# Kernel tuning notes

Measured on AMD Instinct MI355X. Metric: run time of the kernel, lower is better.

The kernel has to match this reference:

```python
import jax, jax.numpy as jnp
import numpy as np

N = 100000
E = 1600000
D_IN = 128
D_HID = 128
D_HID2 = D_HID // 2  # 64
D_OUT = 1


def _glorot(key, shape):
    fan_in, fan_out = shape[1], shape[0]
    lim = float(np.sqrt(6.0 / (fan_in + fan_out)))
    return jax.random.uniform(key, shape, jnp.float32, -lim, lim)


def setup_inputs() -> dict:
    key = jax.random.key(0)
    ks = jax.random.split(key, 10)
    x = jax.random.normal(ks[0], (N, D_IN), jnp.float32)
    edge_index = jax.random.randint(ks[1], (2, E), 0, N, jnp.int64)
    return {
        "x": x,
        "edge_index": edge_index,
        # SAGEConv1: lin_l acts on mean-aggregated neighbors, lin_r on root
        "W1_l": _glorot(ks[2], (D_HID, D_IN)),
        "W1_r": _glorot(ks[3], (D_HID, D_IN)),
        "b1": jnp.zeros((D_HID,), jnp.float32),
        # SAGEConv2
        "W2_l": _glorot(ks[4], (D_HID2, D_HID)),
        "W2_r": _glorot(ks[5], (D_HID2, D_HID)),
        "b2": jnp.zeros((D_HID2,), jnp.float32),
        # classifier Linear
        "Wc": _glorot(ks[6], (D_OUT, D_HID2)),
        "bc": jnp.zeros((D_OUT,), jnp.float32),
    }


def _sage_conv(x, src, dst, Wl, Wr, b):
    # mean aggregation of source features onto destination nodes
    msg = x[src]  # [E, d] gather
    agg = jax.ops.segment_sum(msg, dst, num_segments=x.shape[0])  # [N, d]
    deg = jax.ops.segment_sum(jnp.ones((src.shape[0],), x.dtype), dst,
                              num_segments=x.shape[0])  # [N]
    agg = agg / jnp.maximum(deg, 1.0)[:, None]
    # out = lin_l(mean_aggr) + lin_r(x) + bias  (PyG SAGEConv default)
    return agg @ Wl.T + x @ Wr.T + b


def reference(x, edge_index, W1_l, W1_r, b1, W2_l, W2_r, b2, Wc, bc):
    src, dst = edge_index[0], edge_index[1]
    h = jax.nn.relu(_sage_conv(x, src, dst, W1_l, W1_r, b1))
    # dropout(p=0.3) is identity in eval mode
    h = jax.nn.relu(_sage_conv(h, src, dst, W2_l, W2_r, b2))
    logits = h @ Wc.T + bc  # [N, 1]
    return logits
```

## Files before the change

kernel.cpp:

```cpp
#include <hip/hip_runtime.h>


static constexpr int TPB = 256;
static constexpr int NWG = 512;
static constexpr int ECMAX = 3200;
static constexpr int NBMAX = 1024;

typedef __attribute__((ext_vector_type(8))) short bf16x8;
typedef __attribute__((ext_vector_type(4))) float f32x4;
typedef __attribute__((ext_vector_type(2))) float f32x2;

#if __has_builtin(__builtin_amdgcn_cvt_pk_f32_fp8) && __has_builtin(__builtin_amdgcn_cvt_pk_fp8_f32)
#define FP8_HW 1
#endif

__device__ __forceinline__ unsigned short f2bf(float f) {
  union { float f; unsigned u; } v; v.f = f;
  unsigned r = v.u + 0x7FFFu + ((v.u >> 16) & 1u);
  return (unsigned short)(r >> 16);
}
__device__ __forceinline__ float bf2f(unsigned short h) {
  union { unsigned u; float f; } v; v.u = ((unsigned)h) << 16;
  return v.f;
}

__device__ __forceinline__ float fp82f_sw(unsigned u) {
  unsigned e = (u >> 3) & 15u, m = u & 7u;
  float f;
  if (e == 0) f = (float)m * 0.001953125f;
  else {
    union { unsigned u; float f; } v;
    v.u = ((e + 120u) << 23) | (m << 20);
    f = v.f;
  }
  return (u & 0x80u) ? -f : f;
}

__device__ __forceinline__ unsigned char f2fp8(float f) {
#ifdef FP8_HW
  return (unsigned char)(__builtin_amdgcn_cvt_pk_fp8_f32(f, f, 0, false) & 0xFF);
#else
  union { float f; unsigned u; } v; v.f = f;
  unsigned s = (v.u >> 24) & 0x80u;
  unsigned a = v.u & 0x7FFFFFFFu;
  if (a >= 0x43E00000u) return (unsigned char)(s | 0x7Eu);
  int e32 = (int)(a >> 23);
  if (e32 < 121) {
    float sc = __builtin_fabsf(f) * 512.0f;
    int m = (int)(sc + 0.5f);
    if (m >= 8) return (unsigned char)(s | 0x08u);
    return (unsigned char)(s | (unsigned)m);
  }
  unsigned m = a & 0x7FFFFFu;
  unsigned lsb = (m >> 20) & 1u;
  m += 0x7FFFFu + lsb;
  unsigned e8 = (unsigned)(e32 - 120);
  if (m >= 0x800000u) { m -= 0x800000u; e8 += 1; }
  if (e8 >= 16) return (unsigned char)(s | 0x7Eu);
  return (unsigned char)(s | (e8 << 3) | (m >> 20));
#endif
}

__device__ __forceinline__ void fp8x8_acc(uint2 v, float* acc) {
#ifdef FP8_HW
  f32x2 a0 = __builtin_amdgcn_cvt_pk_f32_fp8(v.x, false);
  f32x2 a1 = __builtin_amdgcn_cvt_pk_f32_fp8(v.x, true);
  f32x2 a2 = __builtin_amdgcn_cvt_pk_f32_fp8(v.y, false);
  f32x2 a3 = __builtin_amdgcn_cvt_pk_f32_fp8(v.y, true);
  acc[0] += a0[0]; acc[1] += a0[1]; acc[2] += a1[0]; acc[3] += a1[1];
  acc[4] += a2[0]; acc[5] += a2[1]; acc[6] += a3[0]; acc[7] += a3[1];
#else
  acc[0] += fp82f_sw(v.x & 255); acc[1] += fp82f_sw((v.x >> 8) & 255);
  acc[2] += fp82f_sw((v.x >> 16) & 255); acc[3] += fp82f_sw(v.x >> 24);
  acc[4] += fp82f_sw(v.y & 255); acc[5] += fp82f_sw((v.y >> 8) & 255);
  acc[6] += fp82f_sw((v.y >> 16) & 255); acc[7] += fp82f_sw(v.y >> 24);
#endif
}

__global__ __launch_bounds__(TPB) void k_bcount(const int* __restrict__ dst,
                                                int* __restrict__ bcnt,
                                                int E, int NB, int EC) {
  extern __shared__ int lhist0[];
  int t = threadIdx.x;
  for (int b = t; b < NB; b += TPB) lhist0[b] = 0;
  __syncthreads();
  int base = blockIdx.x * EC;
  int cnt = min(EC, E - base);
  for (int i = t; i < cnt; i += TPB)
    atomicAdd(&lhist0[dst[base + i] >> 7], 1);
  __syncthreads();
  for (int b = t; b < NB; b += TPB) {
    int c = lhist0[b];
    if (c) atomicAdd(&bcnt[b], c);
  }
}

__global__ __launch_bounds__(TPB) void k_bscatter(
    const int* __restrict__ src, const int* __restrict__ dst,
    const int* __restrict__ bcnt, int* __restrict__ bcur,
    int* __restrict__ ebuf, int E, int NB, int EC) {
  __shared__ int pv[ECMAX];
  __shared__ unsigned short kb[ECMAX];
  __shared__ int sb[NBMAX];
  __shared__ int lhist[NBMAX];
  __shared__ int lcur[NBMAX];
  __shared__ int sp[TPB];
  int t = threadIdx.x;
  int loc[4]; int ssum = 0;
#pragma unroll
  for (int q = 0; q < 4; ++q) {
    int idx = t * 4 + q;
    loc[q] = (idx < NB) ? bcnt[idx] : 0;
    ssum += loc[q];
  }
  sp[t] = ssum; __syncthreads();
  for (int off = 1; off < TPB; off <<= 1) {
    int x = (t >= off) ? sp[t - off] : 0;
    __syncthreads();
    sp[t] += x;
    __syncthreads();
  }
  int run = sp[t] - ssum;
#pragma unroll
  for (int q = 0; q < 4; ++q) {
    int idx = t * 4 + q;
    if (idx < NB) sb[idx] = run;
    run += loc[q];
  }
  for (int b = t; b < NB; b += TPB) lhist[b] = 0;
  int base = blockIdx.x * EC;
  int cnt = min(EC, E - base);
  __syncthreads();
  for (int i = t; i < cnt; i += TPB) {
    int sv = src[base + i], dv = dst[base + i];
    int b = dv >> 7;
    kb[i] = (unsigned short)b;
    pv[i] = ((dv & 127) << 17) | sv;
    atomicAdd(&lhist[b], 1);
  }
  __syncthreads();
  for (int b = t; b < NB; b += TPB) {
    int c = lhist[b];
    lcur[b] = c ? (sb[b] + atomicAdd(&bcur[b], c)) : 0;
  }
  __syncthreads();
  for (int i = t; i < cnt; i += TPB) {
    int b = kb[i];
    int pos = atomicAdd(&lcur[b], 1);
    ebuf[pos] = pv[i];
  }
}

__global__ __launch_bounds__(TPB) void k_bcsr(
    const int* __restrict__ ebuf, const int* __restrict__ bcnt,
    int* __restrict__ rowptr, int* __restrict__ col, int N, int NB) {
  __shared__ int deg[128], sscan[128], lcur[128], red[TPB];
  int b = blockIdx.x, t = threadIdx.x;
  int part = 0;
  for (int i = t; i < b; i += TPB) part += bcnt[i];
  red[t] = part; __syncthreads();
  for (int off = TPB / 2; off > 0; off >>= 1) {
    if (t < off) red[t] += red[t + off];
    __syncthreads();
  }
  int e0 = red[0];
  int e1 = e0 + bcnt[b];
  if (t < 128) deg[t] = 0;
  __syncthreads();
  for (int i = e0 + t; i < e1; i += TPB)
    atomicAdd(&deg[ebuf[i] >> 17], 1);
  __syncthreads();
  if (t < 128) sscan[t] = deg[t];
  __syncthreads();
  for (int off = 1; off < 128; off <<= 1) {
    int x = 0;
    if (t < 128 && t >= off) x = sscan[t - off];
    __syncthreads();
    if (t < 128) sscan[t] += x;
    __syncthreads();
  }
  if (t < 128) {
    int excl = sscan[t] - deg[t];
    int node0 = (b << 7) + t;
    if (node0 < N) rowptr[node0] = e0 + excl;
    lcur[t] = e0 + excl;
  }
  if (b == NB - 1 && t == 0) rowptr[N] = e1;
  __syncthreads();
  for (int i = e0 + t; i < e1; i += TPB) {
    int pvv = ebuf[i];
    int pos = atomicAdd(&lcur[pvv >> 17], 1);
    col[pos] = pvv & 0x1FFFF;
  }
}

static constexpr int LD = 136;

template <bool OUT8>
__device__ __forceinline__ void mfma_tile_128(
    const unsigned short* As, const unsigned short* Bs,
    void* __restrict__ outp, int row0, int N, int w, int l) {
  int lr = l & 15, lk = l >> 4;
  f32x4 acc[4][2];
#pragma unroll
  for (int mb = 0; mb < 4; ++mb)
#pragma unroll
    for (int nb = 0; nb < 2; ++nb)
#pragma unroll
      for (int q = 0; q < 4; ++q) acc[mb][nb][q] = 0.f;
#pragma unroll
  for (int ks = 0; ks < 4; ++ks) {
    int koff = ks * 32 + lk * 8;
    bf16x8 a[4], bfr[2];
#pragma unroll
    for (int mb = 0; mb < 4; ++mb)
      a[mb] = *(const bf16x8*)&As[(mb * 16 + lr) * LD + koff];
#pragma unroll
    for (int nb = 0; nb < 2; ++nb)
      bfr[nb] = *(const bf16x8*)&Bs[(w * 32 + nb * 16 + lr) * LD + koff];
#pragma unroll
    for (int mb = 0; mb < 4; ++mb)
#pragma unroll
      for (int nb = 0; nb < 2; ++nb)
        acc[mb][nb] = __builtin_amdgcn_mfma_f32_16x16x32_bf16(a[mb], bfr[nb], acc[mb][nb], 0, 0, 0);
  }
#pragma unroll
  for (int mb = 0; mb < 4; ++mb) {
    int r = row0 + mb * 16 + lk * 4;
#pragma unroll
    for (int nb = 0; nb < 2; ++nb) {
      int c = w * 32 + nb * 16 + lr;
#pragma unroll
      for (int j = 0; j < 4; ++j) {
        if (r + j < N) {
          if (OUT8) ((unsigned char*)outp)[(size_t)(r + j) * 128 + c] = f2fp8(acc[mb][nb][j]);
          else      ((unsigned short*)outp)[(size_t)(r + j) * 128 + c] = f2bf(acc[mb][nb][j]);
        }
      }
    }
  }
}

__global__ __launch_bounds__(TPB) void k_lin1d(
    const float* __restrict__ X, const float* __restrict__ W1l,
    const float* __restrict__ W1r, unsigned char* __restrict__ t1,
    unsigned short* __restrict__ r1, int N) {
  __shared__ unsigned short Bs[128 * LD];
  __shared__ unsigned short As[64 * LD];
  int t = threadIdx.x;
  int row0 = blockIdx.x * 64;
  for (int i = t; i < 64 * 32; i += TPB) {
    int r = i >> 5, k4 = i & 31;
    int gr = row0 + r;
    float4 v;
    if (gr < N) v = *(const float4*)&X[(size_t)gr * 128 + k4 * 4];
    else { v.x = v.y = v.z = v.w = 0.f; }
    ushort4 o; o.x = f2bf(v.x); o.y = f2bf(v.y); o.z = f2bf(v.z); o.w = f2bf(v.w);
    *(ushort4*)&As[r * LD + k4 * 4] = o;
  }
  for (int i = t; i < 128 * 32; i += TPB) {
    int r = i >> 5, k4 = i & 31;
    float4 v = *(const float4*)&W1l[r * 128 + k4 * 4];
    ushort4 o; o.x = f2bf(v.x); o.y = f2bf(v.y); o.z = f2bf(v.z); o.w = f2bf(v.w);
    *(ushort4*)&Bs[r * LD + k4 * 4] = o;
  }
  __syncthreads();
  int w = t >> 6, l = t & 63;
  mfma_tile_128<true>(As, Bs, t1, row0, N, w, l);
  __syncthreads();
  for (int i = t; i < 128 * 32; i += TPB) {
    int r = i >> 5, k4 = i & 31;
    float4 v = *(const float4*)&W1r[r * 128 + k4 * 4];
    ushort4 o; o.x = f2bf(v.x); o.y = f2bf(v.y); o.z = f2bf(v.z); o.w = f2bf(v.w);
    *(ushort4*)&Bs[r * LD + k4 * 4] = o;
  }
  __syncthreads();
  mfma_tile_128<false>(As, Bs, r1, row0, N, w, l);
}

__global__ void k_aggh1(const unsigned char* __restrict__ t1,
                        const unsigned short* __restrict__ r1,
                        const int* __restrict__ rowptr, const int* __restrict__ col,
                        const float* __restrict__ b1,
                        unsigned short* __restrict__ h1, int n) {
  int wid = (int)(((size_t)blockIdx.x * blockDim.x + threadIdx.x) >> 6);
  int l = threadIdx.x & 63;
  if (wid >= n) return;
  int rp0 = rowptr[wid], rp1 = rowptr[wid + 1];
  int g = l >> 4, s = l & 15;
  float acc[8];
#pragma unroll
  for (int q = 0; q < 8; ++q) acc[q] = 0.f;
  int j = rp0 + g;
  for (; j + 12 < rp1; j += 16) {
    int c0 = col[j], c1 = col[j + 4], c2 = col[j + 8], c3 = col[j + 12];
    uint2 v0 = *(const uint2*)&t1[(size_t)c0 * 128 + s * 8];
    uint2 v1 = *(const uint2*)&t1[(size_t)c1 * 128 + s * 8];
    uint2 v2 = *(const uint2*)&t1[(size_t)c2 * 128 + s * 8];
    uint2 v3 = *(const uint2*)&t1[(size_t)c3 * 128 + s * 8];
    fp8x8_acc(v0, acc); fp8x8_acc(v1, acc);
    fp8x8_acc(v2, acc); fp8x8_acc(v3, acc);
  }
  for (; j + 4 < rp1; j += 8) {
    int c0 = col[j], c1 = col[j + 4];
    uint2 v0 = *(const uint2*)&t1[(size_t)c0 * 128 + s * 8];
    uint2 v1 = *(const uint2*)&t1[(size_t)c1 * 128 + s * 8];
    fp8x8_acc(v0, acc); fp8x8_acc(v1, acc);
  }
  if (j < rp1) {
    uint2 v0 = *(const uint2*)&t1[(size_t)col[j] * 128 + s * 8];
    fp8x8_acc(v0, acc);
  }
#pragma unroll
  for (int q = 0; q < 8; ++q) {
    acc[q] += __shfl_xor(acc[q], 16, 64);
    acc[q] += __shfl_xor(acc[q], 32, 64);
  }
  if (g == 0) {
    int d = rp1 - rp0;
    float inv = 1.f / (float)(d > 1 ? d : 1);
    bf16x8 rr = *(const bf16x8*)&r1[(size_t)wid * 128 + s * 8];
    float4 bb0 = *(const float4*)&b1[s * 8];
    float4 bb1 = *(const float4*)&b1[s * 8 + 4];
    float bbv[8] = {bb0.x, bb0.y, bb0.z, bb0.w, bb1.x, bb1.y, bb1.z, bb1.w};
    bf16x8 o;
#pragma unroll
    for (int q = 0; q < 8; ++q) {
      float h = acc[q] * inv + bf2f((unsigned short)rr[q]) + bbv[q];
      h = h > 0.f ? h : 0.f;
      o[q] = (short)f2bf(h);
    }
    *(bf16x8*)&h1[(size_t)wid * 128 + s * 8] = o;
  }
}

__global__ __launch_bounds__(TPB) void k_lin2(
    const unsigned short* __restrict__ h1,
    const float* __restrict__ W2l, const float* __restrict__ W2r,
    unsigned char* __restrict__ y2, unsigned short* __restrict__ r2, int N) {
  __shared__ unsigned short Bs[128 * LD];
  __shared__ unsigned short As[64 * LD];
  int t = threadIdx.x;
  for (int i = t; i < 128 * 32; i += TPB) {
    int r = i >> 5, k4 = i & 31;
    const float* srcp = (r < 64) ? &W2l[(size_t)r * 128 + k4 * 4]
                                 : &W2r[(size_t)(r - 64) * 128 + k4 * 4];
    float4 v = *(const float4*)srcp;
    ushort4 o; o.x = f2bf(v.x); o.y = f2bf(v.y); o.z = f2bf(v.z); o.w = f2bf(v.w);
    *(ushort4*)&Bs[r * LD + k4 * 4] = o;
  }
  int row0 = blockIdx.x * 64;
  for (int i = t * 8; i < 64 * 128; i += TPB * 8) {
    int r = i >> 7, k8 = i & 127;
    int gr = row0 + r;
    bf16x8 v;
    if (gr < N) v = *(const bf16x8*)&h1[(size_t)gr * 128 + k8];
    else { for (int q = 0; q < 8; ++q) v[q] = 0; }
    *(bf16x8*)&As[r * LD + k8] = v;
  }
  __syncthreads();
  int w = t >> 6, l = t & 63;
  int lr = l & 15, lk = l >> 4;
  f32x4 acc[4][2];
#pragma unroll
  for (int mb = 0; mb < 4; ++mb)
#pragma unroll
    for (int nb = 0; nb < 2; ++nb)
#pragma unroll
      for (int q = 0; q < 4; ++q) acc[mb][nb][q] = 0.f;
#pragma unroll
  for (int ks = 0; ks < 4; ++ks) {
    int koff = ks * 32 + lk * 8;
    bf16x8 a[4], bfr[2];
#pragma unroll
    for (int mb = 0; mb < 4; ++mb)
      a[mb] = *(const bf16x8*)&As[(mb * 16 + lr) * LD + koff];
#pragma unroll
    for (int nb = 0; nb < 2; ++nb)
      bfr[nb] = *(const bf16x8*)&Bs[(w * 32 + nb * 16 + lr) * LD + koff];
#pragma unroll
    for (int mb = 0; mb < 4; ++mb)
#pragma unroll
      for (int nb = 0; nb < 2; ++nb)
        acc[mb][nb] = __builtin_amdgcn_mfma_f32_16x16x32_bf16(a[mb], bfr[nb], acc[mb][nb], 0, 0, 0);
  }
#pragma unroll
  for (int mb = 0; mb < 4; ++mb) {
    int r = row0 + mb * 16 + lk * 4;
#pragma unroll
    for (int nb = 0; nb < 2; ++nb) {
      int c = w * 32 + nb * 16 + lr;
#pragma unroll
      for (int j = 0; j < 4; ++j) {
        if (r + j < N) {
          if (c < 64) y2[(size_t)(r + j) * 64 + c] = f2fp8(acc[mb][nb][j]);
          else        r2[(size_t)(r + j) * 64 + (c - 64)] = f2bf(acc[mb][nb][j]);
        }
      }
    }
  }
}

__global__ void k_agghead(const unsigned char* __restrict__ y2,
                          const unsigned short* __restrict__ r2,
                          const int* __restrict__ rowptr, const int* __restrict__ col,
                          const float* __restrict__ b2, const float* __restrict__ Wc,
                          const float* __restrict__ bc, float* __restrict__ out, int n) {
  int wid = (int)(((size_t)blockIdx.x * blockDim.x + threadIdx.x) >> 6);
  int l = threadIdx.x & 63;
  if (wid >= n) return;
  int rp0 = rowptr[wid], rp1 = rowptr[wid + 1];
  int g = l >> 3, s = l & 7;
  float acc[8];
#pragma unroll
  for (int q = 0; q < 8; ++q) acc[q] = 0.f;
  int j = rp0 + g;
  for (; j + 8 < rp1; j += 16) {
    int c0 = col[j], c1 = col[j + 8];
    uint2 v0 = *(const uint2*)&y2[(size_t)c0 * 64 + s * 8];
    uint2 v1 = *(const uint2*)&y2[(size_t)c1 * 64 + s * 8];
    fp8x8_acc(v0, acc); fp8x8_acc(v1, acc);
  }
  if (j < rp1) {
    uint2 v0 = *(const uint2*)&y2[(size_t)col[j] * 64 + s * 8];
    fp8x8_acc(v0, acc);
  }
#pragma unroll
  for (int q = 0; q < 8; ++q) {
    acc[q] += __shfl_xor(acc[q], 8, 64);
    acc[q] += __shfl_xor(acc[q], 16, 64);
    acc[q] += __shfl_xor(acc[q], 32, 64);
  }
  if (g == 0) {
    int d = rp1 - rp0;
    float inv = 1.f / (float)(d > 1 ? d : 1);
    bf16x8 rr = *(const bf16x8*)&r2[(size_t)wid * 64 + s * 8];
    float4 bb0 = *(const float4*)&b2[s * 8];
    float4 bb1 = *(const float4*)&b2[s * 8 + 4];
    float bbv[8] = {bb0.x, bb0.y, bb0.z, bb0.w, bb1.x, bb1.y, bb1.z, bb1.w};
    float4 wc0 = *(const float4*)&Wc[s * 8];
    float4 wc1 = *(const float4*)&Wc[s * 8 + 4];
    float wcv[8] = {wc0.x, wc0.y, wc0.z, wc0.w, wc1.x, wc1.y, wc1.z, wc1.w};
    float p = 0.f;
#pragma unroll
    for (int q = 0; q < 8; ++q) {
      float h = acc[q] * inv + bf2f((unsigned short)rr[q]) + bbv[q];
      h = h > 0.f ? h : 0.f;
      p += h * wcv[q];
    }
    p += __shfl_xor(p, 1, 64);
    p += __shfl_xor(p, 2, 64);
    p += __shfl_xor(p, 4, 64);
    if (s == 0) out[wid] = p + bc[0];
  }
}

extern "C" void kernel_launch(void* const* d_in, const int* in_sizes, int n_in,
                              void* d_out, int out_size, void* d_ws, size_t ws_size,
                              hipStream_t stream) {
  const float* x   = (const float*)d_in[0];
  const int*   ei  = (const int*)d_in[1];
  const float* W1l = (const float*)d_in[2];
  const float* W1r = (const float*)d_in[3];
  const float* b1  = (const float*)d_in[4];
  const float* W2l = (const float*)d_in[5];
  const float* W2r = (const float*)d_in[6];
  const float* b2  = (const float*)d_in[7];
  const float* Wc  = (const float*)d_in[8];
  const float* bc  = (const float*)d_in[9];
  float* logits = (float*)d_out;

  const int N = in_sizes[0] / 128;
  const int E = in_sizes[1] / 2;
  const int NB = (N + 127) >> 7;
  const int EC = (E + NWG - 1) / NWG;

  char* ws = (char*)d_ws;
  size_t o = 0;
  auto alloc = [&](size_t bytes) { size_t r = o; o += (bytes + 511) & ~511ULL; return r; };
  size_t o_rp    = alloc((size_t)(N + 1) * 4);
  size_t o_bcc   = alloc((size_t)(2 * NB) * 4);
  size_t o_col   = alloc((size_t)E * 4);
  size_t o_ebuf  = alloc((size_t)E * 4);
  size_t o_t1    = alloc((size_t)N * 128);
  size_t o_r1    = alloc((size_t)N * 128 * 2);
  size_t o_h1    = alloc((size_t)N * 128 * 2);
  size_t o_y2    = alloc((size_t)N * 64);
  size_t o_r2    = alloc((size_t)N * 64 * 2);
  if (o > ws_size) return;

  int* rp    = (int*)(ws + o_rp);
  int* bcnt  = (int*)(ws + o_bcc);
  int* bcur  = bcnt + NB;
  int* col   = (int*)(ws + o_col);
  int* ebuf  = (int*)(ws + o_ebuf);
  unsigned char*  t1 = (unsigned char*)(ws + o_t1);
  unsigned short* r1 = (unsigned short*)(ws + o_r1);
  unsigned short* h1 = (unsigned short*)(ws + o_h1);
  unsigned char*  y2 = (unsigned char*)(ws + o_y2);
  unsigned short* r2 = (unsigned short*)(ws + o_r2);

  const int* esrc = ei;
  const int* edst = ei + E;

  int gtiles = (N + 63) / 64;
  int nodeblocks = (int)(((size_t)N * 64 + TPB - 1) / TPB);

  hipMemsetAsync(bcnt, 0, (size_t)(2 * NB) * 4, stream);
  k_bcount<<<NWG, TPB, (size_t)NB * 4, stream>>>(edst, bcnt, E, NB, EC);
  k_lin1d<<<gtiles, TPB, 0, stream>>>(x, W1l, W1r, t1, r1, N);
  k_bscatter<<<NWG, TPB, 0, stream>>>(esrc, edst, bcnt, bcur, ebuf, E, NB, EC);
  k_bcsr<<<NB, TPB, 0, stream>>>(ebuf, bcnt, rp, col, N, NB);
  k_aggh1<<<nodeblocks, TPB, 0, stream>>>(t1, r1, rp, col, b1, h1, N);
  k_lin2<<<gtiles, TPB, 0, stream>>>(h1, W2l, W2r, y2, r2, N);
  k_agghead<<<nodeblocks, TPB, 0, stream>>>(y2, r2, rp, col, b2, Wc, bc, logits, N);
}
```

Before: 227.0 us.

## Pre-convert weights to bf16 once and read B fragments from global

Adds a small prep kernel that converts all layer weights to bf16 once per call, instead of every GEMM block re-reading fp32 weights and converting them into shared memory. The lin1 and lin2 kernels drop the weight shared-memory tile and load B fragments straight from global/L2. lin1 also computes both projections in one pass over the A fragments, with two accumulator sets. This is meant to cut redundant per-block weight conversion and LDS traffic and raise occupancy, at the cost of one extra launch, more registers in lin1 and uncoalesced global fragment loads.

```diff
diff --git a/kernel.cpp b/kernel.cpp
--- a/kernel.cpp
+++ b/kernel.cpp
@@ -77,6 +77,18 @@
 #endif
 }
 
+__global__ void k_wprep(const float* __restrict__ W1l, const float* __restrict__ W1r,
+                        const float* __restrict__ W2l, const float* __restrict__ W2r,
+                        unsigned short* __restrict__ wb1l,
+                        unsigned short* __restrict__ wb1r,
+                        unsigned short* __restrict__ wb2) {
+  int i = blockIdx.x * blockDim.x + threadIdx.x;
+  if (i < 16384) wb1l[i] = f2bf(W1l[i]);
+  else if (i < 32768) wb1r[i - 16384] = f2bf(W1r[i - 16384]);
+  else if (i < 40960) wb2[i - 32768] = f2bf(W2l[i - 32768]);
+  else if (i < 49152) wb2[8192 + i - 40960] = f2bf(W2r[i - 40960]);
+}
+
 __global__ __launch_bounds__(TPB) void k_bcount(const int* __restrict__ dst,
                                                 int* __restrict__ bcnt,
                                                 int E, int NB, int EC) {
@@ -196,56 +208,10 @@
 
 static constexpr int LD = 136;
 
-template <bool OUT8>
-__device__ __forceinline__ void mfma_tile_128(
-    const unsigned short* As, const unsigned short* Bs,
-    void* __restrict__ outp, int row0, int N, int w, int l) {
-  int lr = l & 15, lk = l >> 4;
-  f32x4 acc[4][2];
-#pragma unroll
-  for (int mb = 0; mb < 4; ++mb)
-#pragma unroll
-    for (int nb = 0; nb < 2; ++nb)
-#pragma unroll
-      for (int q = 0; q < 4; ++q) acc[mb][nb][q] = 0.f;
-#pragma unroll
-  for (int ks = 0; ks < 4; ++ks) {
-    int koff = ks * 32 + lk * 8;
-    bf16x8 a[4], bfr[2];
-#pragma unroll
-    for (int mb = 0; mb < 4; ++mb)
-      a[mb] = *(const bf16x8*)&As[(mb * 16 + lr) * LD + koff];
-#pragma unroll
-    for (int nb = 0; nb < 2; ++nb)
-      bfr[nb] = *(const bf16x8*)&Bs[(w * 32 + nb * 16 + lr) * LD + koff];
-#pragma unroll
-    for (int mb = 0; mb < 4; ++mb)
-#pragma unroll
-      for (int nb = 0; nb < 2; ++nb)
-        acc[mb][nb] = __builtin_amdgcn_mfma_f32_16x16x32_bf16(a[mb], bfr[nb], acc[mb][nb], 0, 0, 0);
-  }
-#pragma unroll
-  for (int mb = 0; mb < 4; ++mb) {
-    int r = row0 + mb * 16 + lk * 4;
-#pragma unroll
-    for (int nb = 0; nb < 2; ++nb) {
-      int c = w * 32 + nb * 16 + lr;
-#pragma unroll
-      for (int j = 0; j < 4; ++j) {
-        if (r + j < N) {
-          if (OUT8) ((unsigned char*)outp)[(size_t)(r + j) * 128 + c] = f2fp8(acc[mb][nb][j]);
-          else      ((unsigned short*)outp)[(size_t)(r + j) * 128 + c] = f2bf(acc[mb][nb][j]);
-        }
-      }
-    }
-  }
-}
-
-__global__ __launch_bounds__(TPB) void k_lin1d(
-    const float* __restrict__ X, const float* __restrict__ W1l,
-    const float* __restrict__ W1r, unsigned char* __restrict__ t1,
+__global__ __launch_bounds__(TPB, 4) void k_lin1(
+    const float* __restrict__ X, const unsigned short* __restrict__ wl,
+    const unsigned short* __restrict__ wr, unsigned char* __restrict__ t1,
     unsigned short* __restrict__ r1, int N) {
-  __shared__ unsigned short Bs[128 * LD];
   __shared__ unsigned short As[64 * LD];
   int t = threadIdx.x;
   int row0 = blockIdx.x * 64;
@@ -258,24 +224,111 @@
     ushort4 o; o.x = f2bf(v.x); o.y = f2bf(v.y); o.z = f2bf(v.z); o.w = f2bf(v.w);
     *(ushort4*)&As[r * LD + k4 * 4] = o;
   }
-  for (int i = t; i < 128 * 32; i += TPB) {
-    int r = i >> 5, k4 = i & 31;
-    float4 v = *(const float4*)&W1l[r * 128 + k4 * 4];
-    ushort4 o; o.x = f2bf(v.x); o.y = f2bf(v.y); o.z = f2bf(v.z); o.w = f2bf(v.w);
-    *(ushort4*)&Bs[r * LD + k4 * 4] = o;
-  }
   __syncthreads();
   int w = t >> 6, l = t & 63;
-  mfma_tile_128<true>(As, Bs, t1, row0, N, w, l);
-  __syncthreads();
-  for (int i = t; i < 128 * 32; i += TPB) {
-    int r = i >> 5, k4 = i & 31;
-    float4 v = *(const float4*)&W1r[r * 128 + k4 * 4];
-    ushort4 o; o.x = f2bf(v.x); o.y = f2bf(v.y); o.z = f2bf(v.z); o.w = f2bf(v.w);
-    *(ushort4*)&Bs[r * LD + k4 * 4] = o;
-  }
-  __syncthreads();
-  mfma_tile_128<false>(As, Bs, r1, row0, N, w, l);
+  int lr = l & 15, lk = l >> 4;
+  f32x4 at[4][2], ar[4][2];
+#pragma unroll
+  for (int mb = 0; mb < 4; ++mb)
+#pragma unroll
+    for (int nb = 0; nb < 2; ++nb)
+#pragma unroll
+      for (int q = 0; q < 4; ++q) { at[mb][nb][q] = 0.f; ar[mb][nb][q] = 0.f; }
+#pragma unroll
+  for (int ks = 0; ks < 4; ++ks) {
+    int koff = ks * 32 + lk * 8;
+    bf16x8 a[4], bl[2], br[2];
+#pragma unroll
+    for (int mb = 0; mb < 4; ++mb)
+      a[mb] = *(const bf16x8*)&As[(mb * 16 + lr) * LD + koff];
+#pragma unroll
+    for (int nb = 0; nb < 2; ++nb) {
+      int c = w * 32 + nb * 16 + lr;
+      bl[nb] = *(const bf16x8*)&wl[c * 128 + koff];
+      br[nb] = *(const bf16x8*)&wr[c * 128 + koff];
+    }
+#pragma unroll
+    for (int mb = 0; mb < 4; ++mb)
+#pragma unroll
+      for (int nb = 0; nb < 2; ++nb) {
+        at[mb][nb] = __builtin_amdgcn_mfma_f32_16x16x32_bf16(a[mb], bl[nb], at[mb][nb], 0, 0, 0);
+        ar[mb][nb] = __builtin_amdgcn_mfma_f32_16x16x32_bf16(a[mb], br[nb], ar[mb][nb], 0, 0, 0);
+      }
+  }
+#pragma unroll
+  for (int mb = 0; mb < 4; ++mb) {
+    int r = row0 + mb * 16 + lk * 4;
+#pragma unroll
+    for (int nb = 0; nb < 2; ++nb) {
+      int c = w * 32 + nb * 16 + lr;
+#pragma unroll
+      for (int j = 0; j < 4; ++j) {
+        if (r + j < N) {
+          t1[(size_t)(r + j) * 128 + c] = f2fp8(at[mb][nb][j]);
+          r1[(size_t)(r + j) * 128 + c] = f2bf(ar[mb][nb][j]);
+        }
+      }
+    }
+  }
+}
+
+__global__ __launch_bounds__(TPB, 4) void k_lin2(
+    const unsigned short* __restrict__ h1, const unsigned short* __restrict__ w2,
+    unsigned char* __restrict__ y2, unsigned short* __restrict__ r2, int N) {
+  __shared__ unsigned short As[64 * LD];
+  int t = threadIdx.x;
+  int row0 = blockIdx.x * 64;
+  for (int i = t * 8; i < 64 * 128; i += TPB * 8) {
+    int r = i >> 7, k8 = i & 127;
+    int gr = row0 + r;
+    bf16x8 v;
+    if (gr < N) v = *(const bf16x8*)&h1[(size_t)gr * 128 + k8];
+    else { for (int q = 0; q < 8; ++q) v[q] = 0; }
+    *(bf16x8*)&As[r * LD + k8] = v;
+  }
+  __syncthreads();
+  int w = t >> 6, l = t & 63;
+  int lr = l & 15, lk = l >> 4;
+  f32x4 acc[4][2];
+#pragma unroll
+  for (int mb = 0; mb < 4; ++mb)
+#pragma unroll
+    for (int nb = 0; nb < 2; ++nb)
+#pragma unroll
+      for (int q = 0; q < 4; ++q) acc[mb][nb][q] = 0.f;
+#pragma unroll
+  for (int ks = 0; ks < 4; ++ks) {
+    int koff = ks * 32 + lk * 8;
+    bf16x8 a[4], bfr[2];
+#pragma unroll
+    for (int mb = 0; mb < 4; ++mb)
+      a[mb] = *(const bf16x8*)&As[(mb * 16 + lr) * LD + koff];
+#pragma unroll
+    for (int nb = 0; nb < 2; ++nb) {
+      int c = w * 32 + nb * 16 + lr;
+      bfr[nb] = *(const bf16x8*)&w2[c * 128 + koff];
+    }
+#pragma unroll
+    for (int mb = 0; mb < 4; ++mb)
+#pragma unroll
+      for (int nb = 0; nb < 2; ++nb)
+        acc[mb][nb] = __builtin_amdgcn_mfma_f32_16x16x32_bf16(a[mb], bfr[nb], acc[mb][nb], 0, 0, 0);
+  }
+#pragma unroll
+  for (int mb = 0; mb < 4; ++mb) {
+    int r = row0 + mb * 16 + lk * 4;
+#pragma unroll
+    for (int nb = 0; nb < 2; ++nb) {
+      int c = w * 32 + nb * 16 + lr;
+#pragma unroll
+      for (int j = 0; j < 4; ++j) {
+        if (r + j < N) {
+          if (c < 64) y2[(size_t)(r + j) * 64 + c] = f2fp8(acc[mb][nb][j]);
+          else        r2[(size_t)(r + j) * 64 + (c - 64)] = f2bf(acc[mb][nb][j]);
+        }
+      }
+    }
+  }
 }
 
 __global__ void k_aggh1(const unsigned char* __restrict__ t1,
@@ -331,73 +384,6 @@
       o[q] = (short)f2bf(h);
     }
     *(bf16x8*)&h1[(size_t)wid * 128 + s * 8] = o;
-  }
-}
-
-__global__ __launch_bounds__(TPB) void k_lin2(
-    const unsigned short* __restrict__ h1,
-    const float* __restrict__ W2l, const float* __restrict__ W2r,
-    unsigned char* __restrict__ y2, unsigned short* __restrict__ r2, int N) {
-  __shared__ unsigned short Bs[128 * LD];
-  __shared__ unsigned short As[64 * LD];
-  int t = threadIdx.x;
-  for (int i = t; i < 128 * 32; i += TPB) {
-    int r = i >> 5, k4 = i & 31;
-    const float* srcp = (r < 64) ? &W2l[(size_t)r * 128 + k4 * 4]
-                                 : &W2r[(size_t)(r - 64) * 128 + k4 * 4];
-    float4 v = *(const float4*)srcp;
-    ushort4 o; o.x = f2bf(v.x); o.y = f2bf(v.y); o.z = f2bf(v.z); o.w = f2bf(v.w);
-    *(ushort4*)&Bs[r * LD + k4 * 4] = o;
-  }
-  int row0 = blockIdx.x * 64;
-  for (int i = t * 8; i < 64 * 128; i += TPB * 8) {
-    int r = i >> 7, k8 = i & 127;
-    int gr = row0 + r;
-    bf16x8 v;
-    if (gr < N) v = *(const bf16x8*)&h1[(size_t)gr * 128 + k8];
-    else { for (int q = 0; q < 8; ++q) v[q] = 0; }
-    *(bf16x8*)&As[r * LD + k8] = v;
-  }
-  __syncthreads();
-  int w = t >> 6, l = t & 63;
-  int lr = l & 15, lk = l >> 4;
-  f32x4 acc[4][2];
-#pragma unroll
-  for (int mb = 0; mb < 4; ++mb)
-#pragma unroll
-    for (int nb = 0; nb < 2; ++nb)
-#pragma unroll
-      for (int q = 0; q < 4; ++q) acc[mb][nb][q] = 0.f;
-#pragma unroll
-  for (int ks = 0; ks < 4; ++ks) {
-    int koff = ks * 32 + lk * 8;
-    bf16x8 a[4], bfr[2];
-#pragma unroll
-    for (int mb = 0; mb < 4; ++mb)
-      a[mb] = *(const bf16x8*)&As[(mb * 16 + lr) * LD + koff];
-#pragma unroll
-    for (int nb = 0; nb < 2; ++nb)
-      bfr[nb] = *(const bf16x8*)&Bs[(w * 32 + nb * 16 + lr) * LD + koff];
-#pragma unroll
-    for (int mb = 0; mb < 4; ++mb)
-#pragma unroll
-      for (int nb = 0; nb < 2; ++nb)
-        acc[mb][nb] = __builtin_amdgcn_mfma_f32_16x16x32_bf16(a[mb], bfr[nb], acc[mb][nb], 0, 0, 0);
-  }
-#pragma unroll
-  for (int mb = 0; mb < 4; ++mb) {
-    int r = row0 + mb * 16 + lk * 4;
-#pragma unroll
-    for (int nb = 0; nb < 2; ++nb) {
-      int c = w * 32 + nb * 16 + lr;
-#pragma unroll
-      for (int j = 0; j < 4; ++j) {
-        if (r + j < N) {
-          if (c < 64) y2[(size_t)(r + j) * 64 + c] = f2fp8(acc[mb][nb][j]);
-          else        r2[(size_t)(r + j) * 64 + (c - 64)] = f2bf(acc[mb][nb][j]);
-        }
-      }
-    }
   }
 }
 
@@ -482,6 +468,7 @@
   size_t o_bcc   = alloc((size_t)(2 * NB) * 4);
   size_t o_col   = alloc((size_t)E * 4);
   size_t o_ebuf  = alloc((size_t)E * 4);
+  size_t o_wb    = alloc((size_t)(3 * 128 * 128) * 2);
   size_t o_t1    = alloc((size_t)N * 128);
   size_t o_r1    = alloc((size_t)N * 128 * 2);
   size_t o_h1    = alloc((size_t)N * 128 * 2);
@@ -494,6 +481,9 @@
   int* bcur  = bcnt + NB;
   int* col   = (int*)(ws + o_col);
   int* ebuf  = (int*)(ws + o_ebuf);
+  unsigned short* wb1l = (unsigned short*)(ws + o_wb);
+  unsigned short* wb1r = wb1l + 128 * 128;
+  unsigned short* wb2  = wb1r + 128 * 128;
   unsigned char*  t1 = (unsigned char*)(ws + o_t1);
   unsigned short* r1 = (unsigned short*)(ws + o_r1);
   unsigned short* h1 = (unsigned short*)(ws + o_h1);
@@ -507,11 +497,12 @@
   int nodeblocks = (int)(((size_t)N * 64 + TPB - 1) / TPB);
 
   hipMemsetAsync(bcnt, 0, (size_t)(2 * NB) * 4, stream);
+  k_wprep<<<192, TPB, 0, stream>>>(W1l, W1r, W2l, W2r, wb1l, wb1r, wb2);
   k_bcount<<<NWG, TPB, (size_t)NB * 4, stream>>>(edst, bcnt, E, NB, EC);
-  k_lin1d<<<gtiles, TPB, 0, stream>>>(x, W1l, W1r, t1, r1, N);
+  k_lin1<<<gtiles, TPB, 0, stream>>>(x, wb1l, wb1r, t1, r1, N);
   k_bscatter<<<NWG, TPB, 0, stream>>>(esrc, edst, bcnt, bcur, ebuf, E, NB, EC);
   k_bcsr<<<NB, TPB, 0, stream>>>(ebuf, bcnt, rp, col, N, NB);
   k_aggh1<<<nodeblocks, TPB, 0, stream>>>(t1, r1, rp, col, b1, h1, N);
-  k_lin2<<<gtiles, TPB, 0, stream>>>(h1, W2l, W2r, y2, r2, N);
+  k_lin2<<<gtiles, TPB, 0, stream>>>(h1, wb2, y2, r2, N);
   k_agghead<<<nodeblocks, TPB, 0, stream>>>(y2, r2, rp, col, b2, Wc, bc, logits, N);
 }
```

After: 213.6 us. 1.06x faster.
